# Performance work log

Measured on AMD Instinct MI355X. Metric: run time of the kernel, lower is better.

## Reference

```python
import jax, jax.numpy as jnp
import numpy as np

B_SZ, D, H, W = 32, 96, 64, 64
N = 4            # d_state
R = 6            # dt_rank = ceil(96/16)
K = 5            # d_conv
EPS = 1e-9
LOG_EPS = float(np.log(EPS))


def setup_inputs() -> dict:
    key = jax.random.key(0)
    ks = jax.random.split(key, 8)
    x = jax.random.normal(ks[0], (B_SZ, D, H, W), dtype=jnp.float32)
    conv_w = jax.random.normal(ks[1], (D, 1, K, K), dtype=jnp.float32) * (1.0 / K)
    conv_b = jax.random.normal(ks[2], (D,), dtype=jnp.float32) * 0.02
    x_proj_w = jax.random.normal(ks[3], (R + 2 * N, D), dtype=jnp.float32) * (D ** -0.5)
    dt_w = jax.random.uniform(ks[4], (D, R), dtype=jnp.float32, minval=-(R ** -0.5), maxval=R ** -0.5)
    # dt bias init: inverse-softplus of dt ~ U(log 1e-3, log 1e-1)
    dt = jnp.exp(jax.random.uniform(ks[5], (D,), dtype=jnp.float32) * (np.log(0.1) - np.log(0.001)) + np.log(0.001))
    dt = jnp.clip(dt, 1e-4, None)
    dt_b = dt + jnp.log(-jnp.expm1(-dt))
    A_logs = jnp.log(jnp.broadcast_to(jnp.arange(1, N + 1, dtype=jnp.float32), (D, N)))
    Ds = jnp.ones((D,), dtype=jnp.float32)
    return {"x": x, "conv_w": conv_w, "conv_b": conv_b, "x_proj_w": x_proj_w,
            "dt_w": dt_w, "dt_b": dt_b, "A_logs": A_logs, "Ds": Ds}


def _forward(x, conv_w, conv_b, x_proj_w, dt_w, dt_b, A_logs, Ds):
    B, C, h, w = x.shape
    L = h * w
    # depthwise conv2d, padding='same' for odd kernel, + SiLU
    x = jax.lax.conv_general_dilated(
        x, conv_w, window_strides=(1, 1), padding=((K // 2, K // 2), (K // 2, K // 2)),
        dimension_numbers=("NCHW", "OIHW", "NCHW"), feature_group_count=C)
    x = x + conv_b[None, :, None, None]
    x = jax.nn.silu(x)
    xs = x.reshape(B, C, L)                                  # [B, D, L]
    x_dbl = jnp.einsum("kd,bdl->bkl", x_proj_w, xs)          # [B, R+2N, L]
    dts, Bs, Cs = x_dbl[:, :R], x_dbl[:, R:R + N], x_dbl[:, R + N:]
    delta = jax.nn.softplus(jnp.einsum("dr,brl->bdl", dt_w, dts) + dt_b[None, :, None])
    A = -jnp.exp(A_logs)                                     # [D, N]
    # log(dA.clamp(min=EPS)) with dA = exp(delta * A)  ==  max(delta*A, log EPS)
    log_dA = jnp.maximum(delta[:, :, None, :] * A[None, :, :, None], LOG_EPS)  # [B,D,N,L]
    P = jnp.exp(jnp.cumsum(log_dA, axis=-1))                 # [B,D,N,L]
    dB_u = delta[:, :, None, :] * Bs[:, None, :, :] * xs[:, :, None, :]        # [B,D,N,L]
    hs = P * jnp.cumsum(dB_u / jnp.maximum(P, EPS), axis=-1)  # state trajectory
    y = jnp.einsum("bdnl,bnl->bdl", hs, Cs) + xs * Ds[None, :, None]
    return y.reshape(B, C, h, w)


def reference(x, conv_w, conv_b, x_proj_w, dt_w, dt_b, A_logs, Ds):
    return _forward(x, conv_w, conv_b, x_proj_w, dt_w, dt_b, A_logs, Ds)
```

## Files before the change

### kernel.cpp

```cpp
#include <hip/hip_runtime.h>

#define B_SZ 32
#define D_CH 96
#define L_SZ 4096
#define N_ST 4
#define R_RK 6

static __device__ __forceinline__ float softplus_f(float v) {
    return fmaxf(v, 0.0f) + __logf(1.0f + __expf(-fabsf(v)));
}

static __device__ __forceinline__ float exp2_fast(float x) {
#if __has_builtin(__builtin_amdgcn_exp2f)
    return __builtin_amdgcn_exp2f(x);
#else
    return __expf(x * 0.6931471805599453f);
#endif
}

template<int CTRL, int RMASK>
static __device__ __forceinline__ float dpp_add(float v) {
    const int t = __builtin_amdgcn_update_dpp(0, __float_as_int(v),
                                              CTRL, RMASK, 0xf, true);
    return v + __int_as_float(t);
}

static __device__ __forceinline__ float wave_incl_scan(float v) {
    v = dpp_add<0x111, 0xf>(v);
    v = dpp_add<0x112, 0xf>(v);
    v = dpp_add<0x114, 0xf>(v);
    v = dpp_add<0x118, 0xf>(v);
    v = dpp_add<0x142, 0xa>(v);
    v = dpp_add<0x143, 0xc>(v);
    return v;
}

static __device__ __forceinline__ float block_excl_scan(float v, float* slot, int t)
{
    const int lane = t & 63;
    const int wid  = t >> 6;
    const float incl = wave_incl_scan(v);
    if (lane == 63) slot[wid] = incl;
    const float ex = incl - v;
    __syncthreads();
    float wp = 0.0f;
#pragma unroll
    for (int w = 0; w < 7; ++w)
        if (w < wid) wp += slot[w];
    return wp + ex;
}

#define TS 76
__global__ __launch_bounds__(256) void conv_silu_kernel(
    const float* __restrict__ x, const float* __restrict__ conv_w,
    const float* __restrict__ conv_b, float* __restrict__ xs)
{
    __shared__ float tile[68 * TS];
    const int t = threadIdx.x;
    const int bd = blockIdx.x;
    const int d = bd % D_CH;
    const float* img = x + bd * L_SZ;

    float wreg[25];
#pragma unroll
    for (int i = 0; i < 25; ++i) wreg[i] = conv_w[d * 25 + i];
    const float bias = conv_b[d];

    const float4 z4 = make_float4(0.f, 0.f, 0.f, 0.f);
    for (int i = t; i < 68 * TS / 4; i += 256) ((float4*)tile)[i] = z4;
    __syncthreads();
    for (int i = t; i < 1024; i += 256) {
        const int r = i >> 4;
        const int c = (i & 15) << 2;
        const float4 v = *(const float4*)(img + (r << 6) + c);
        *(float4*)(tile + (r + 2) * TS + 4 + c) = v;
    }
    __syncthreads();

    const int hr = t >> 2;
    const int cb = (t & 3) << 4;

    float acc[16];
#pragma unroll
    for (int j = 0; j < 16; ++j) acc[j] = bias;

#pragma unroll
    for (int kh = 0; kh < 5; ++kh) {
        const float* rp = tile + (hr + kh) * TS + cb;
        float r24[24];
#pragma unroll
        for (int q = 0; q < 6; ++q) {
            const float4 v = ((const float4*)rp)[q];
            r24[4*q+0] = v.x; r24[4*q+1] = v.y; r24[4*q+2] = v.z; r24[4*q+3] = v.w;
        }
#pragma unroll
        for (int j = 0; j < 16; ++j)
#pragma unroll
            for (int kw = 0; kw < 5; ++kw)
                acc[j] += wreg[kh * 5 + kw] * r24[j + kw + 2];
    }

    float* out = xs + bd * L_SZ + (hr << 6) + cb;
#pragma unroll
    for (int q = 0; q < 4; ++q) {
        float4 v;
#pragma unroll
        for (int j = 0; j < 4; ++j) {
            const float a = acc[4*q + j];
            const float s = __builtin_amdgcn_rcpf(1.0f + __expf(-a));
            (&v.x)[j] = a * s;
        }
        ((float4*)out)[q] = v;
    }
}

__global__ __launch_bounds__(256) void proj_kernel(
    const float* __restrict__ xs, const float* __restrict__ x_proj_w,
    float* __restrict__ x_dbl)
{
    __shared__ float red[4][14][64];
    const int t = threadIdx.x;
    const int g = t >> 6;
    const int ll = t & 63;
    const int bi = blockIdx.x;
    const int b = bi >> 6;
    const int chunk = bi & 63;
    const int l = (chunk << 6) + ll;
    const int d0 = __builtin_amdgcn_readfirstlane(g * 24);

    const float* xsb = xs + (b * D_CH + d0) * L_SZ + l;
    float acc[14];
#pragma unroll
    for (int k = 0; k < 14; ++k) acc[k] = 0.0f;

#pragma unroll
    for (int dd = 0; dd < 24; ++dd) {
        const float xv = xsb[dd * L_SZ];
#pragma unroll
        for (int k = 0; k < 14; ++k)
            acc[k] += x_proj_w[k * D_CH + d0 + dd] * xv;
    }

#pragma unroll
    for (int k = 0; k < 14; ++k) red[g][k][ll] = acc[k];
    __syncthreads();

    float* outb = x_dbl + b * 14 * L_SZ + (chunk << 6);
    for (int i = t; i < 14 * 64; i += 256) {
        const int k = i >> 6;
        const int c = i & 63;
        outb[k * L_SZ + c] = red[0][k][c] + red[1][k][c] + red[2][k][c] + red[3][k][c];
    }
}

__global__ __launch_bounds__(512, 4) void scan_kernel(
    const float* __restrict__ xs, const float* __restrict__ x_dbl,
    const float* __restrict__ dt_w, const float* __restrict__ dt_b,
    const float* __restrict__ A_logs, const float* __restrict__ Ds,
    float* __restrict__ y)
{
    constexpr float L2EPS = -29.897352853986263f;
    constexpr float L2E   = 1.4426950408889634f;

    __shared__ float slots[8][8];
    const int t = threadIdx.x;
    const int bd = blockIdx.x;
    const int b = bd / D_CH;
    const int d = bd - b * D_CH;
    const int l0 = t * 8;

    const float* xs_row = xs + bd * L_SZ + l0;
    const float* xd = x_dbl + b * 14 * L_SZ + l0;

    float xv[8];
#pragma unroll
    for (int i = 0; i < 2; ++i) {
        const float4 v = ((const float4*)xs_row)[i];
        xv[4*i+0] = v.x; xv[4*i+1] = v.y; xv[4*i+2] = v.z; xv[4*i+3] = v.w;
    }

    const float dtb = dt_b[d];
    float dl[8];
#pragma unroll
    for (int i = 0; i < 8; ++i) dl[i] = dtb;
#pragma unroll
    for (int r = 0; r < R_RK; ++r) {
        const float wr = dt_w[d * R_RK + r];
        const float* row = xd + r * L_SZ;
#pragma unroll
        for (int i = 0; i < 2; ++i) {
            const float4 v = ((const float4*)row)[i];
            dl[4*i+0] += wr * v.x; dl[4*i+1] += wr * v.y;
            dl[4*i+2] += wr * v.z; dl[4*i+3] += wr * v.w;
        }
    }
#pragma unroll
    for (int i = 0; i < 8; ++i) dl[i] = softplus_f(dl[i]);

    const float dsd = Ds[d];
    float dlxv[8], yac[8];
#pragma unroll
    for (int i = 0; i < 8; ++i) { dlxv[i] = dl[i] * xv[i]; yac[i] = xv[i] * dsd; }

    for (int n = 0; n < N_ST; ++n) {
        const float An2 = -__expf(A_logs[d * N_ST + n]) * L2E;

        float SP[8];
        float run = 0.0f;
#pragma unroll
        for (int i = 0; i < 8; ++i) {
            run += fmaxf(dl[i] * An2, L2EPS);
            SP[i] = run;
        }
        const float ex1 = block_excl_scan(run, slots[2*n], t);

        const float* Brow = xd + (R_RK + n) * L_SZ;
        float carr[8];
        float run2 = 0.0f;
#pragma unroll
        for (int i = 0; i < 2; ++i) {
            const float4 v = ((const float4*)Brow)[i];
            const float bb[4] = {v.x, v.y, v.z, v.w};
#pragma unroll
            for (int j = 0; j < 4; ++j) {
                const int idx = 4*i + j;
                const float S = SP[idx] + ex1;
                const float e = exp2_fast(-S);
                const float pinv = fminf(e, 1e9f);
                SP[idx] = __builtin_amdgcn_rcpf(e);
                run2 = fmaf(dlxv[idx] * bb[j], pinv, run2);
                carr[idx] = run2;
            }
        }
        const float ex2 = block_excl_scan(run2, slots[2*n+1], t);

        const float* Crow = xd + (R_RK + N_ST + n) * L_SZ;
#pragma unroll
        for (int i = 0; i < 2; ++i) {
            const float4 v = ((const float4*)Crow)[i];
            const float cc[4] = {v.x, v.y, v.z, v.w};
#pragma unroll
            for (int j = 0; j < 4; ++j) {
                const int idx = 4*i + j;
                yac[idx] = fmaf(SP[idx] * (carr[idx] + ex2), cc[j], yac[idx]);
            }
        }
    }

    float* yrow = y + bd * L_SZ + l0;
#pragma unroll
    for (int i = 0; i < 2; ++i) {
        float4 v;
        v.x = yac[4*i+0]; v.y = yac[4*i+1];
        v.z = yac[4*i+2]; v.w = yac[4*i+3];
        ((float4*)yrow)[i] = v;
    }
}

extern "C" void kernel_launch(void* const* d_in, const int* in_sizes, int n_in,
                              void* d_out, int out_size, void* d_ws, size_t ws_size,
                              hipStream_t stream)
{
    const float* x        = (const float*)d_in[0];
    const float* conv_w   = (const float*)d_in[1];
    const float* conv_b   = (const float*)d_in[2];
    const float* x_proj_w = (const float*)d_in[3];
    const float* dt_w     = (const float*)d_in[4];
    const float* dt_b     = (const float*)d_in[5];
    const float* A_logs   = (const float*)d_in[6];
    const float* Ds       = (const float*)d_in[7];

    float* y     = (float*)d_out;
    float* xs    = y;
    float* x_dbl = (float*)d_ws;

    conv_silu_kernel<<<B_SZ * D_CH, 256, 0, stream>>>(x, conv_w, conv_b, xs);
    proj_kernel<<<B_SZ * 64, 256, 0, stream>>>(xs, x_proj_w, x_dbl);
    scan_kernel<<<B_SZ * D_CH, 512, 0, stream>>>(xs, x_dbl, dt_w, dt_b,
                                                 A_logs, Ds, y);
}
```

Before: 84.10 us.

## Fuse depthwise conv+SiLU with x_proj projection in one row-per-block kernel

Merges the conv+SiLU kernel and the projection kernel into one kernel where each block handles one image row across all 96 channels. Conv inputs are read straight from global memory with boundary predication instead of a padded shared tile. The SiLU outputs are transposed into shared memory so the 14-row projection runs without re-reading xs from global. This removes one launch and the xs re-read, at the cost of the conv losing shared-memory reuse (5x redundant row loads hitting cache) and a different, swizzled block mapping.

```diff
diff --git a/kernel.cpp b/kernel.cpp
--- a/kernel.cpp
+++ b/kernel.cpp
@@ -50,35 +50,26 @@
     return wp + ex;
 }
 
-#define TS 76
-__global__ __launch_bounds__(256) void conv_silu_kernel(
+__global__ __launch_bounds__(384) void conv_proj_kernel(
     const float* __restrict__ x, const float* __restrict__ conv_w,
-    const float* __restrict__ conv_b, float* __restrict__ xs)
-{
-    __shared__ float tile[68 * TS];
+    const float* __restrict__ conv_b, const float* __restrict__ x_proj_w,
+    float* __restrict__ xs, float* __restrict__ x_dbl)
+{
+    __shared__ float smT[64][100];
     const int t = threadIdx.x;
-    const int bd = blockIdx.x;
-    const int d = bd % D_CH;
-    const float* img = x + bd * L_SZ;
-
-    float wreg[25];
-#pragma unroll
-    for (int i = 0; i < 25; ++i) wreg[i] = conv_w[d * 25 + i];
-    const float bias = conv_b[d];
-
+    const int s = ((blockIdx.x & 7) << 8) + (blockIdx.x >> 3);
+    const int b = s >> 6;
+    const int r = s & 63;
+
+    const int ch   = t >> 2;
+    const int g    = t & 3;
+    const int col0 = g << 4;
+    const float* img = x + (b * D_CH + ch) * L_SZ;
+    const float* wbase = conv_w + ch * 25;
+    const float bias = conv_b[ch];
+    const bool gok0 = (g != 0);
+    const bool gok5 = (g != 3);
     const float4 z4 = make_float4(0.f, 0.f, 0.f, 0.f);
-    for (int i = t; i < 68 * TS / 4; i += 256) ((float4*)tile)[i] = z4;
-    __syncthreads();
-    for (int i = t; i < 1024; i += 256) {
-        const int r = i >> 4;
-        const int c = (i & 15) << 2;
-        const float4 v = *(const float4*)(img + (r << 6) + c);
-        *(float4*)(tile + (r + 2) * TS + 4 + c) = v;
-    }
-    __syncthreads();
-
-    const int hr = t >> 2;
-    const int cb = (t & 3) << 4;
 
     float acc[16];
 #pragma unroll
@@ -86,70 +77,80 @@
 
 #pragma unroll
     for (int kh = 0; kh < 5; ++kh) {
-        const float* rp = tile + (hr + kh) * TS + cb;
+        const int rr = r - 2 + kh;
+        const bool rowok = (rr >= 0) && (rr < 64);
+        const float* rowp = img + (rr << 6) + col0 - 4;
+        float wrow[5];
+#pragma unroll
+        for (int kw = 0; kw < 5; ++kw) wrow[kw] = wbase[kh * 5 + kw];
+
         float r24[24];
 #pragma unroll
         for (int q = 0; q < 6; ++q) {
-            const float4 v = ((const float4*)rp)[q];
+            const bool ok = rowok && (q == 0 ? gok0 : (q == 5 ? gok5 : true));
+            const float4 v = ok ? ((const float4*)rowp)[q] : z4;
             r24[4*q+0] = v.x; r24[4*q+1] = v.y; r24[4*q+2] = v.z; r24[4*q+3] = v.w;
         }
 #pragma unroll
         for (int j = 0; j < 16; ++j)
 #pragma unroll
             for (int kw = 0; kw < 5; ++kw)
-                acc[j] += wreg[kh * 5 + kw] * r24[j + kw + 2];
-    }
-
-    float* out = xs + bd * L_SZ + (hr << 6) + cb;
+                acc[j] += wrow[kw] * r24[j + kw + 2];
+    }
+
+#pragma unroll
+    for (int j = 0; j < 16; ++j) {
+        const float a = acc[j];
+        acc[j] = a * __builtin_amdgcn_rcpf(1.0f + __expf(-a));
+    }
+    float* outg = xs + (b * D_CH + ch) * L_SZ + (r << 6) + col0;
 #pragma unroll
     for (int q = 0; q < 4; ++q) {
         float4 v;
-#pragma unroll
-        for (int j = 0; j < 4; ++j) {
-            const float a = acc[4*q + j];
-            const float s = __builtin_amdgcn_rcpf(1.0f + __expf(-a));
-            (&v.x)[j] = a * s;
-        }
-        ((float4*)out)[q] = v;
-    }
-}
-
-__global__ __launch_bounds__(256) void proj_kernel(
-    const float* __restrict__ xs, const float* __restrict__ x_proj_w,
-    float* __restrict__ x_dbl)
-{
-    __shared__ float red[4][14][64];
-    const int t = threadIdx.x;
-    const int g = t >> 6;
-    const int ll = t & 63;
-    const int bi = blockIdx.x;
-    const int b = bi >> 6;
-    const int chunk = bi & 63;
-    const int l = (chunk << 6) + ll;
-    const int d0 = __builtin_amdgcn_readfirstlane(g * 24);
-
-    const float* xsb = xs + (b * D_CH + d0) * L_SZ + l;
-    float acc[14];
-#pragma unroll
-    for (int k = 0; k < 14; ++k) acc[k] = 0.0f;
-
-#pragma unroll
-    for (int dd = 0; dd < 24; ++dd) {
-        const float xv = xsb[dd * L_SZ];
-#pragma unroll
-        for (int k = 0; k < 14; ++k)
-            acc[k] += x_proj_w[k * D_CH + d0 + dd] * xv;
-    }
-
-#pragma unroll
-    for (int k = 0; k < 14; ++k) red[g][k][ll] = acc[k];
+        v.x = acc[4*q+0]; v.y = acc[4*q+1]; v.z = acc[4*q+2]; v.w = acc[4*q+3];
+        ((float4*)outg)[q] = v;
+    }
+#pragma unroll
+    for (int j = 0; j < 16; ++j)
+        smT[col0 + j][ch] = acc[j];
+
     __syncthreads();
 
-    float* outb = x_dbl + b * 14 * L_SZ + (chunk << 6);
-    for (int i = t; i < 14 * 64; i += 256) {
-        const int k = i >> 6;
-        const int c = i & 63;
-        outb[k * L_SZ + c] = red[0][k][c] + red[1][k][c] + red[2][k][c] + red[3][k][c];
+    const int px = t & 63;
+    const int kk = __builtin_amdgcn_readfirstlane(t >> 6);
+    const float* srow = &smT[px][0];
+    float* xdb = x_dbl + (b * 14) * L_SZ + (r << 6) + px;
+    const float* w0 = x_proj_w + (kk    ) * D_CH;
+    const float* w1 = x_proj_w + (kk + 6) * D_CH;
+
+    if (kk < 2) {
+        const float* w2 = x_proj_w + (kk + 12) * D_CH;
+        float a0 = 0.f, a1 = 0.f, a2 = 0.f;
+#pragma unroll
+        for (int c = 0; c < D_CH; c += 4) {
+            const float4 sv = *(const float4*)(srow + c);
+            a0 = fmaf(sv.x, w0[c+0], a0); a0 = fmaf(sv.y, w0[c+1], a0);
+            a0 = fmaf(sv.z, w0[c+2], a0); a0 = fmaf(sv.w, w0[c+3], a0);
+            a1 = fmaf(sv.x, w1[c+0], a1); a1 = fmaf(sv.y, w1[c+1], a1);
+            a1 = fmaf(sv.z, w1[c+2], a1); a1 = fmaf(sv.w, w1[c+3], a1);
+            a2 = fmaf(sv.x, w2[c+0], a2); a2 = fmaf(sv.y, w2[c+1], a2);
+            a2 = fmaf(sv.z, w2[c+2], a2); a2 = fmaf(sv.w, w2[c+3], a2);
+        }
+        xdb[(kk     ) * L_SZ] = a0;
+        xdb[(kk +  6) * L_SZ] = a1;
+        xdb[(kk + 12) * L_SZ] = a2;
+    } else {
+        float a0 = 0.f, a1 = 0.f;
+#pragma unroll
+        for (int c = 0; c < D_CH; c += 4) {
+            const float4 sv = *(const float4*)(srow + c);
+            a0 = fmaf(sv.x, w0[c+0], a0); a0 = fmaf(sv.y, w0[c+1], a0);
+            a0 = fmaf(sv.z, w0[c+2], a0); a0 = fmaf(sv.w, w0[c+3], a0);
+            a1 = fmaf(sv.x, w1[c+0], a1); a1 = fmaf(sv.y, w1[c+1], a1);
+            a1 = fmaf(sv.z, w1[c+2], a1); a1 = fmaf(sv.w, w1[c+3], a1);
+        }
+        xdb[(kk    ) * L_SZ] = a0;
+        xdb[(kk + 6) * L_SZ] = a1;
     }
 }
 
@@ -274,8 +275,8 @@
     float* xs    = y;
     float* x_dbl = (float*)d_ws;
 
-    conv_silu_kernel<<<B_SZ * D_CH, 256, 0, stream>>>(x, conv_w, conv_b, xs);
-    proj_kernel<<<B_SZ * 64, 256, 0, stream>>>(xs, x_proj_w, x_dbl);
+    conv_proj_kernel<<<B_SZ * 64, 384, 0, stream>>>(x, conv_w, conv_b,
+                                                    x_proj_w, xs, x_dbl);
     scan_kernel<<<B_SZ * D_CH, 512, 0, stream>>>(xs, x_dbl, dt_w, dt_b,
                                                  A_logs, Ds, y);
 }
```

Result: slower. 180.3 us (+114.4%).
